# Kernel tuning notes

Hardware: AMD Instinct MI355X
Metric: run time of the kernel (lower is better)

The kernel has to match this reference:

```python
import jax, jax.numpy as jnp
from jax import lax
import numpy as np

B = 8; L = 1024; D_MODEL = 128; N_LAYER = 4
D_INNER = 256; D_STATE = 16; D_CONV = 4; DT_RANK = 8  # ceil(128/16)
N_STATE = 2; EPS = 1e-5


def setup_inputs() -> dict:
    key = jax.random.key(0)
    ks = jax.random.split(key, 9)
    s = 0.02
    return {
        "x": jax.random.normal(ks[0], (B, L, D_MODEL), jnp.float32),
        "in_proj_w": jax.random.normal(ks[1], (N_LAYER, 2 * D_INNER, D_MODEL), jnp.float32) * s,
        "conv_w": jax.random.normal(ks[2], (N_LAYER, D_INNER, 1, D_CONV), jnp.float32) * s,
        "conv_b": jnp.zeros((N_LAYER, D_INNER), jnp.float32),
        "x_proj_w": jax.random.normal(ks[3], (N_LAYER, DT_RANK + 2 * D_STATE, D_INNER), jnp.float32) * s,
        "dt_proj_w": jax.random.normal(ks[4], (N_LAYER, D_INNER, DT_RANK), jnp.float32) * s,
        "dt_proj_b": jax.random.normal(ks[5], (N_LAYER, D_INNER), jnp.float32) * s,
        "A_log": jnp.log(jnp.tile(jnp.arange(1, D_STATE + 1, dtype=jnp.float32), (N_LAYER, D_INNER, 1))),
        "D_param": jnp.ones((N_LAYER, D_INNER), jnp.float32),
        "out_proj_w": jax.random.normal(ks[6], (N_LAYER, D_MODEL, D_INNER), jnp.float32) * s,
        "norm_w": jnp.ones((N_LAYER, D_MODEL), jnp.float32),
        "norm_f_w": jnp.ones((D_MODEL,), jnp.float32),
        "bn_gamma": jnp.ones((D_MODEL,), jnp.float32),
        "bn_beta": jnp.zeros((D_MODEL,), jnp.float32),
        "head_w": jax.random.normal(ks[7], (N_STATE, D_MODEL), jnp.float32) * s,
        "head_b": jnp.zeros((N_STATE,), jnp.float32),
    }


def _rmsnorm(x, w):
    return x * lax.rsqrt(jnp.mean(x * x, axis=-1, keepdims=True) + EPS) * w


def _selective_scan(u, delta, A, Bm, Cm, D):
    # u, delta: (b,l,d); A: (d,n); Bm, Cm: (b,l,n); D: (d,)
    deltaA = jnp.exp(delta[..., None] * A)                          # (b,l,d,n)
    deltaBu = delta[..., None] * Bm[:, :, None, :] * u[..., None]   # (b,l,d,n)

    def step(h, t):
        dA, dBu, c = t
        h = dA * h + dBu                                            # (b,d,n)
        return h, jnp.einsum('bdn,bn->bd', h, c)

    h0 = jnp.zeros((u.shape[0], u.shape[2], A.shape[1]), u.dtype)
    _, ys = lax.scan(step, h0, (jnp.moveaxis(deltaA, 1, 0),
                                jnp.moveaxis(deltaBu, 1, 0),
                                jnp.moveaxis(Cm, 1, 0)))
    return jnp.moveaxis(ys, 0, 1) + u * D                           # (b,l,d)


def _mamba_block(x, in_w, cw, cb, xp_w, dt_w, dt_b, A_log, Dp, out_w):
    xz = jnp.einsum('bld,ed->ble', x, in_w)                         # (b,l,2*d_inner)
    xs, res = jnp.split(xz, 2, axis=-1)
    # depthwise causal conv, kernel D_CONV, left pad D_CONV-1 (matches pad=3 + truncate)
    xc = lax.conv_general_dilated(jnp.transpose(xs, (0, 2, 1)), cw, (1,),
                                  [(D_CONV - 1, 0)],
                                  dimension_numbers=('NCH', 'OIH', 'NCH'),
                                  feature_group_count=D_INNER)
    xs = jax.nn.silu(jnp.transpose(xc + cb[None, :, None], (0, 2, 1)))
    dbc = jnp.einsum('bld,ed->ble', xs, xp_w)
    dlt, Bm, Cm = jnp.split(dbc, [DT_RANK, DT_RANK + D_STATE], axis=-1)
    delta = jax.nn.softplus(jnp.einsum('blr,dr->bld', dlt, dt_w) + dt_b)
    A = -jnp.exp(A_log)
    y = _selective_scan(xs, delta, A, Bm, Cm, Dp)
    y = y * jax.nn.silu(res)
    return jnp.einsum('ble,de->bld', y, out_w)


def reference(x, in_proj_w, conv_w, conv_b, x_proj_w, dt_proj_w, dt_proj_b,
              A_log, D_param, out_proj_w, norm_w, norm_f_w,
              bn_gamma, bn_beta, head_w, head_b):
    h = x
    for i in range(N_LAYER):
        h = h + _mamba_block(_rmsnorm(h, norm_w[i]), in_proj_w[i], conv_w[i],
                             conv_b[i], x_proj_w[i], dt_proj_w[i], dt_proj_b[i],
                             A_log[i], D_param[i], out_proj_w[i])
    h = _rmsnorm(h, norm_f_w)
    feat = h[:, -1, :]                                              # (b, d_model)
    # BatchNorm1d (training mode: batch stats, biased variance), ReLU, Dropout(eval)=id
    mu = jnp.mean(feat, axis=0)
    var = jnp.mean((feat - mu) ** 2, axis=0)
    feat = (feat - mu) * lax.rsqrt(var + EPS) * bn_gamma + bn_beta
    feat = jax.nn.relu(feat)
    return feat @ head_w.T + head_b                                 # (b, n_state)
```

## Files before the change

kernel.cpp:

```cpp
#include <hip/hip_runtime.h>
#include <cstddef>

#define LQ 1024
#define DM 128
#define DI 256
#define DSN 16
#define NB 8
#define ROWS (NB*LQ)
#define EPSF 1e-5f
#define CHUNK 32
#define NCHUNK (LQ/CHUNK)

typedef _Float16 f16;
typedef __attribute__((ext_vector_type(8))) _Float16 f16x8;
typedef __attribute__((ext_vector_type(4))) _Float16 f16x4;
typedef __attribute__((ext_vector_type(4))) float f32x4;

static __device__ __forceinline__ float sigmoid_f(float x) { return 1.f/(1.f+__expf(-x)); }
static __device__ __forceinline__ float softplus_f(float x) {
  return (x > 20.f) ? x : log1pf(__expf(x));
}

__global__ __launch_bounds__(256) void cvt_all(
    const float* __restrict__ a, const float* __restrict__ bsrc, const float* __restrict__ csrc,
    f16* __restrict__ oa, f16* __restrict__ ob, f16* __restrict__ oc)
{
  int i = blockIdx.x*256 + threadIdx.x;
  const int na = (4*2*DI*DM)/4;
  const int nb = (4*40*DI)/4;
  const int nc = (4*DM*DI)/4;
  const float* s; f16* o; int k;
  if (i < na)            { s = a;    o = oa; k = i; }
  else if (i < na+nb)    { s = bsrc; o = ob; k = i - na; }
  else if (i < na+nb+nc) { s = csrc; o = oc; k = i - na - nb; }
  else return;
  float4 v = ((const float4*)s)[k];
  f16x4 r; r.x=(f16)v.x; r.y=(f16)v.y; r.z=(f16)v.z; r.w=(f16)v.w;
  ((f16x4*)o)[k] = r;
}

__global__ __launch_bounds__(256) void norm_inproj(
    const float* __restrict__ hin, const float* __restrict__ nw,
    const f16* __restrict__ Wf, f16* __restrict__ xz)
{
  __shared__ __align__(16) f16 Alds[64][136];
  __shared__ __align__(16) f16 Blds[64][136];
  const int tid = threadIdx.x;
  const int row0 = blockIdx.x*64, col0 = blockIdx.y*64;
  #pragma unroll
  for (int cc = tid; cc < 1024; cc += 256) {
    int r = cc >> 4, off = (cc & 15) << 3;
    *(f16x8*)&Blds[r][off] = *(const f16x8*)(Wf + (size_t)(col0 + r)*DM + off);
  }
  {
    const int r = tid >> 2, seg = (tid & 3) * 32;
    const float* hr = hin + (size_t)(row0 + r)*DM + seg;
    float4 v[8];
    float ss = 0.f;
    #pragma unroll
    for (int j = 0; j < 8; ++j) {
      v[j] = *(const float4*)(hr + j*4);
      ss += v[j].x*v[j].x + v[j].y*v[j].y + v[j].z*v[j].z + v[j].w*v[j].w;
    }
    ss += __shfl_xor(ss, 1);
    ss += __shfl_xor(ss, 2);
    const float sc = rsqrtf(ss*(1.f/128.f) + EPSF);
    #pragma unroll
    for (int j = 0; j < 8; ++j) {
      float4 wv = *(const float4*)(nw + seg + j*4);
      f16x4 o;
      o.x = (f16)(v[j].x*sc*wv.x);
      o.y = (f16)(v[j].y*sc*wv.y);
      o.z = (f16)(v[j].z*sc*wv.z);
      o.w = (f16)(v[j].w*sc*wv.w);
      *(f16x4*)&Alds[r][seg + j*4] = o;
    }
  }
  __syncthreads();
  const int l = tid & 63, w = tid >> 6;
  const int wr = w >> 1, wc = w & 1;
  const int fr = l & 15, kg = l >> 4;
  f16x8 af[2][4], bf[2][4];
  #pragma unroll
  for (int m = 0; m < 2; ++m)
    #pragma unroll
    for (int s = 0; s < 4; ++s)
      af[m][s] = *(const f16x8*)&Alds[wr*32 + m*16 + fr][s*32 + kg*8];
  #pragma unroll
  for (int n = 0; n < 2; ++n)
    #pragma unroll
    for (int s = 0; s < 4; ++s)
      bf[n][s] = *(const f16x8*)&Blds[wc*32 + n*16 + fr][s*32 + kg*8];
  f32x4 acc[2][2];
  #pragma unroll
  for (int m = 0; m < 2; ++m)
    #pragma unroll
    for (int n = 0; n < 2; ++n)
      acc[m][n] = (f32x4){0.f,0.f,0.f,0.f};
  #pragma unroll
  for (int s = 0; s < 4; ++s)
    #pragma unroll
    for (int m = 0; m < 2; ++m)
      #pragma unroll
      for (int n = 0; n < 2; ++n)
        acc[m][n] = __builtin_amdgcn_mfma_f32_16x16x32_f16(af[m][s], bf[n][s], acc[m][n], 0, 0, 0);
  #pragma unroll
  for (int m = 0; m < 2; ++m)
    #pragma unroll
    for (int n = 0; n < 2; ++n) {
      const int col = col0 + wc*32 + n*16 + fr;
      #pragma unroll
      for (int j = 0; j < 4; ++j) {
        const int row = row0 + wr*32 + m*16 + kg*4 + j;
        xz[(size_t)row*(2*DI) + col] = (f16)acc[m][n][j];
      }
    }
}

__global__ __launch_bounds__(256) void conv_xproj_p1(
    const f16* __restrict__ xz, const float* __restrict__ cw, const float* __restrict__ cb,
    const f16* __restrict__ xpw, const float* __restrict__ A_log,
    const float* __restrict__ dtw, const float* __restrict__ dtb,
    f16* __restrict__ xs_out, float* __restrict__ dbc_out,
    float* __restrict__ S, float* __restrict__ sumdl_out)
{
  __shared__ __align__(16) f16 sXz[35][256];
  __shared__ __align__(16) f16 sXs[32][264];
  __shared__ __align__(16) f16 sW[48][264];
  __shared__ __align__(16) float sDbc[32][40];
  const int bc = blockIdx.x;
  const int b = bc >> 5, ck = bc & (NCHUNK-1);
  const int t0 = ck*CHUNK;
  const int tid = threadIdx.x;
  for (int e = tid; e < 35*32; e += 256) {
    int r = e >> 5, off = (e & 31) << 3;
    f16x8 v = (f16x8){0,0,0,0,0,0,0,0};
    if (ck > 0 || r >= 3)
      v = *(const f16x8*)(xz + (size_t)(b*LQ + t0 - 3 + r)*(2*DI) + off);
    *(f16x8*)&sXz[r][off] = v;
  }
  for (int e = tid; e < 48*32; e += 256) {
    int r = e >> 5, off = (e & 31) << 3;
    f16x8 v = (f16x8){0,0,0,0,0,0,0,0};
    if (r < 40) v = *(const f16x8*)(xpw + (size_t)r*DI + off);
    *(f16x8*)&sW[r][off] = v;
  }
  __syncthreads();
  {
    const int d = tid;
    const float4 cwv = *(const float4*)(cw + d*4);
    const float bias = cb[d];
    #pragma unroll 4
    for (int t = 0; t < CHUNK; ++t) {
      float acc = bias + (float)sXz[t][d]*cwv.x + (float)sXz[t+1][d]*cwv.y
                       + (float)sXz[t+2][d]*cwv.z + (float)sXz[t+3][d]*cwv.w;
      float sv = acc * sigmoid_f(acc);
      f16 s16 = (f16)sv;
      sXs[t][d] = s16;
      xs_out[(size_t)(b*LQ + t0 + t)*DI + d] = s16;
    }
  }
  __syncthreads();
  const int l = tid & 63, w = tid >> 6;
  const int fr = l & 15, kg = l >> 4;
  if (w < 3) {
    f32x4 acc[2];
    acc[0] = (f32x4){0.f,0.f,0.f,0.f};
    acc[1] = (f32x4){0.f,0.f,0.f,0.f};
    #pragma unroll
    for (int s = 0; s < 8; ++s) {
      f16x8 bfv = *(const f16x8*)&sW[w*16 + fr][s*32 + kg*8];
      #pragma unroll
      for (int m = 0; m < 2; ++m) {
        f16x8 afv = *(const f16x8*)&sXs[m*16 + fr][s*32 + kg*8];
        acc[m] = __builtin_amdgcn_mfma_f32_16x16x32_f16(afv, bfv, acc[m], 0, 0, 0);
      }
    }
    const int col = w*16 + fr;
    if (col < 40) {
      #pragma unroll
      for (int m = 0; m < 2; ++m)
        #pragma unroll
        for (int j = 0; j < 4; ++j) {
          int row = m*16 + kg*4 + j;
          sDbc[row][col] = acc[m][j];
          dbc_out[(size_t)(b*LQ + t0 + row)*40 + col] = acc[m][j];
        }
    }
  }
  __syncthreads();
  {
    const int d = tid;
    float A[16];
    #pragma unroll
    for (int n = 0; n < 16; ++n) A[n] = -__expf(A_log[d*16+n]);
    const float4 dw0 = *(const float4*)(dtw + d*8);
    const float4 dw1 = *(const float4*)(dtw + d*8 + 4);
    const float bt = dtb[d];
    float h[16] = {};
    float sdl = 0.f;
    for (int t = 0; t < CHUNK; ++t) {
      float xa = bt + sDbc[t][0]*dw0.x + sDbc[t][1]*dw0.y + sDbc[t][2]*dw0.z + sDbc[t][3]*dw0.w
                    + sDbc[t][4]*dw1.x + sDbc[t][5]*dw1.y + sDbc[t][6]*dw1.z + sDbc[t][7]*dw1.w;
      float dl = softplus_f(xa);
      float uu = (float)sXs[t][d];
      float du = dl*uu;
      sdl += dl;
      #pragma unroll
      for (int n = 0; n < 16; ++n)
        h[n] = __expf(dl*A[n])*h[n] + du*sDbc[t][8+n];
    }
    float* Sp = S + ((size_t)bc*DI + d)*16;
    #pragma unroll
    for (int n = 0; n < 16; n += 4)
      *(float4*)(Sp+n) = make_float4(h[n],h[n+1],h[n+2],h[n+3]);
    sumdl_out[(size_t)bc*DI + d] = sdl;
  }
}

__global__ __launch_bounds__(256) void scan_p2(
    float* __restrict__ S, const float* __restrict__ sumdl,
    const float* __restrict__ A_log)
{
  int g = blockIdx.x*256 + threadIdx.x;
  int b = g >> 12;
  int dn = g & 4095;
  float A = -__expf(A_log[dn]);
  int d = dn >> 4;
  float H = 0.f;
  for (int c = 0; c < NCHUNK; ++c) {
    size_t cidx = (size_t)(b*NCHUNK + c)*DI + d;
    size_t idx = cidx*16 + (dn & 15);
    float Sv = S[idx];
    float P = __expf(A * sumdl[cidx]);
    S[idx] = H;
    H = P*H + Sv;
  }
}

__global__ __launch_bounds__(256) void p3_outproj(
    const f16* __restrict__ xs, const float* __restrict__ dbc,
    const float* __restrict__ A_log, const float* __restrict__ dtw,
    const float* __restrict__ dtb, const float* __restrict__ Dp,
    const float* __restrict__ Hinit, const f16* __restrict__ xz,
    const f16* __restrict__ Wo, const float* __restrict__ addsrc,
    float* __restrict__ hout)
{
  __shared__ __align__(16) f16 sY[32][264];
  __shared__ float sB[CHUNK][16];
  __shared__ float sC[CHUNK][16];
  __shared__ float sDL[CHUNK][8];
  const int bc = blockIdx.x;
  const int b = bc >> 5, ck = bc & (NCHUNK-1);
  const int t0 = ck*CHUNK;
  const int tid = threadIdx.x;
  for (int e = tid; e < CHUNK*16; e += 256) {
    int t = e >> 4, n = e & 15;
    size_t r = (size_t)(b*LQ + t0 + t)*40;
    sB[t][n] = dbc[r + 8 + n];
    sC[t][n] = dbc[r + 24 + n];
  }
  for (int e = tid; e < CHUNK*8; e += 256) {
    int t = e >> 3, j = e & 7;
    sDL[t][j] = dbc[(size_t)(b*LQ + t0 + t)*40 + j];
  }
  const int d = tid;
  float A[16];
  #pragma unroll
  for (int n = 0; n < 16; ++n) A[n] = -__expf(A_log[d*16+n]);
  const float4 dw0 = *(const float4*)(dtw + d*8);
  const float4 dw1 = *(const float4*)(dtw + d*8 + 4);
  const float bt = dtb[d];
  const float Dv = Dp[d];
  float h[16];
  const float* Hp = Hinit + ((size_t)bc*DI + d)*16;
  #pragma unroll
  for (int n = 0; n < 16; n += 4) {
    float4 v = *(const float4*)(Hp+n);
    h[n]=v.x; h[n+1]=v.y; h[n+2]=v.z; h[n+3]=v.w;
  }
  __syncthreads();
  const size_t ubase = (size_t)(b*LQ + t0)*DI + d;
  const size_t rbase = (size_t)(b*LQ + t0)*(2*DI) + DI + d;
  for (int t = 0; t < CHUNK; ++t) {
    float xa = bt + sDL[t][0]*dw0.x + sDL[t][1]*dw0.y + sDL[t][2]*dw0.z + sDL[t][3]*dw0.w
                  + sDL[t][4]*dw1.x + sDL[t][5]*dw1.y + sDL[t][6]*dw1.z + sDL[t][7]*dw1.w;
    float dl = softplus_f(xa);
    float uu = (float)xs[ubase + (size_t)t*DI];
    float du = dl*uu;
    float acc = uu*Dv;
    #pragma unroll
    for (int n = 0; n < 16; ++n) {
      h[n] = __expf(dl*A[n])*h[n] + du*sB[t][n];
      acc += h[n]*sC[t][n];
    }
    float res = (float)xz[rbase + (size_t)t*(2*DI)];
    sY[t][d] = (f16)(acc * (res * sigmoid_f(res)));
  }
  __syncthreads();
  const int l = tid & 63, w = tid >> 6;
  const int fr = l & 15, kg = l >> 4;
  f16x8 bf[2][8];
  #pragma unroll
  for (int n = 0; n < 2; ++n)
    #pragma unroll
    for (int s = 0; s < 8; ++s)
      bf[n][s] = *(const f16x8*)(Wo + (size_t)(w*32 + n*16 + fr)*DI + s*32 + kg*8);
  f32x4 acc[2][2];
  #pragma unroll
  for (int m = 0; m < 2; ++m)
    #pragma unroll
    for (int n = 0; n < 2; ++n)
      acc[m][n] = (f32x4){0.f,0.f,0.f,0.f};
  #pragma unroll
  for (int s = 0; s < 8; ++s)
    #pragma unroll
    for (int m = 0; m < 2; ++m) {
      f16x8 afv = *(const f16x8*)&sY[m*16 + fr][s*32 + kg*8];
      #pragma unroll
      for (int n = 0; n < 2; ++n)
        acc[m][n] = __builtin_amdgcn_mfma_f32_16x16x32_f16(afv, bf[n][s], acc[m][n], 0, 0, 0);
    }
  #pragma unroll
  for (int m = 0; m < 2; ++m)
    #pragma unroll
    for (int n = 0; n < 2; ++n) {
      const int col = w*32 + n*16 + fr;
      #pragma unroll
      for (int j = 0; j < 4; ++j) {
        const int row = m*16 + kg*4 + j;
        const size_t gi = (size_t)(b*LQ + t0 + row)*DM + col;
        hout[gi] = acc[m][n][j] + addsrc[gi];
      }
    }
}

__global__ __launch_bounds__(256) void final_kernel(const float* __restrict__ h,
    const float* __restrict__ nfw, const float* __restrict__ gamma, const float* __restrict__ beta,
    const float* __restrict__ hw, const float* __restrict__ hb, float* __restrict__ out) {
  __shared__ float sf[8][128];
  __shared__ float sscale[8];
  int tid = threadIdx.x;
  for (int e = tid; e < 1024; e += 256) {
    int b = e >> 7, dd = e & 127;
    sf[b][dd] = h[((size_t)b*LQ + (LQ-1))*DM + dd];
  }
  __syncthreads();
  if (tid < 8) {
    float ss = 0.f;
    for (int dd = 0; dd < 128; ++dd) { float v = sf[tid][dd]; ss += v*v; }
    sscale[tid] = rsqrtf(ss/128.f + EPSF);
  }
  __syncthreads();
  for (int e = tid; e < 1024; e += 256) {
    int b = e >> 7, dd = e & 127;
    sf[b][dd] = sf[b][dd]*sscale[b]*nfw[dd];
  }
  __syncthreads();
  if (tid < 128) {
    float mu = 0.f;
    for (int b = 0; b < 8; ++b) mu += sf[b][tid];
    mu *= 0.125f;
    float var = 0.f;
    for (int b = 0; b < 8; ++b) { float dv = sf[b][tid]-mu; var += dv*dv; }
    var *= 0.125f;
    float rs = rsqrtf(var + EPSF);
    for (int b = 0; b < 8; ++b) {
      float v = (sf[b][tid]-mu)*rs*gamma[tid] + beta[tid];
      sf[b][tid] = v > 0.f ? v : 0.f;
    }
  }
  __syncthreads();
  if (tid < 16) {
    int b = tid >> 1, s = tid & 1;
    float acc = hb[s];
    for (int dd = 0; dd < 128; ++dd) acc += sf[b][dd]*hw[s*128+dd];
    out[b*2+s] = acc;
  }
}

extern "C" void kernel_launch(void* const* d_in, const int* in_sizes, int n_in,
                              void* d_out, int out_size, void* d_ws, size_t ws_size,
                              hipStream_t stream) {
  const float* x      = (const float*)d_in[0];
  const float* in_w   = (const float*)d_in[1];
  const float* conv_w = (const float*)d_in[2];
  const float* conv_b = (const float*)d_in[3];
  const float* xp_w   = (const float*)d_in[4];
  const float* dt_w   = (const float*)d_in[5];
  const float* dt_b   = (const float*)d_in[6];
  const float* A_log  = (const float*)d_in[7];
  const float* Dp     = (const float*)d_in[8];
  const float* out_w  = (const float*)d_in[9];
  const float* norm_w = (const float*)d_in[10];
  const float* norm_f = (const float*)d_in[11];
  const float* gamma  = (const float*)d_in[12];
  const float* beta   = (const float*)d_in[13];
  const float* head_w = (const float*)d_in[14];
  const float* head_b = (const float*)d_in[15];

  float* ws = (float*)d_ws;
  float* h     = ws;
  float* dbc   = h + (size_t)ROWS*DM;
  float* S     = dbc + (size_t)ROWS*40;
  float* sumdl = S + (size_t)NB*NCHUNK*DI*16;
  f16* xz     = (f16*)(sumdl + (size_t)NB*NCHUNK*DI);
  f16* xs     = xz + (size_t)ROWS*2*DI;
  f16* wf_in  = xs + (size_t)ROWS*DI;
  f16* wf_xp  = wf_in + (size_t)4*2*DI*DM;
  f16* wf_out = wf_xp + (size_t)4*40*DI;

  cvt_all<<<424, 256, 0, stream>>>(in_w, xp_w, out_w, wf_in, wf_xp, wf_out);

  for (int layer = 0; layer < 4; ++layer) {
    const float* src = layer ? h : x;
    norm_inproj<<<dim3(ROWS/64, 8), 256, 0, stream>>>(
        src, norm_w + (size_t)layer*DM, wf_in + (size_t)layer*2*DI*DM, xz);
    conv_xproj_p1<<<NB*NCHUNK, 256, 0, stream>>>(
        xz, conv_w + (size_t)layer*DI*4, conv_b + (size_t)layer*DI,
        wf_xp + (size_t)layer*40*DI, A_log + (size_t)layer*DI*DSN,
        dt_w + (size_t)layer*DI*8, dt_b + (size_t)layer*DI,
        xs, dbc, S, sumdl);
    scan_p2<<<NB*DI*DSN/256, 256, 0, stream>>>(S, sumdl, A_log + (size_t)layer*DI*DSN);
    p3_outproj<<<NB*NCHUNK, 256, 0, stream>>>(
        xs, dbc, A_log + (size_t)layer*DI*DSN, dt_w + (size_t)layer*DI*8,
        dt_b + (size_t)layer*DI, Dp + (size_t)layer*DI, S, xz,
        wf_out + (size_t)layer*DM*DI, src, h);
  }
  final_kernel<<<1, 256, 0, stream>>>(h, norm_f, gamma, beta, head_w, head_b, (float*)d_out);
}
```

Measured before the change: 308.3 us.

## Fuse norm and in-projection into scan kernels and drop the chunk-state pass

The separate norm+in-projection kernel is folded into the per-chunk front kernel, which recomputes the x half of the projection for its 35 rows including the conv halo. The back kernel recomputes the z half from the source rows. This removes the global xz buffer write and read. The scan_p2 kernel is removed: each back block serially combines the chunk-end states of all earlier chunks to build its own initial state. In exchange there is redundant halo and projection compute, a serial loop of up to 31 chunks per block, and fewer, heavier blocks in place of the wide standalone GEMM.

```diff
diff --git a/kernel.cpp b/kernel.cpp
--- a/kernel.cpp
+++ b/kernel.cpp
@@ -39,156 +39,141 @@
   ((f16x4*)o)[k] = r;
 }
 
-__global__ __launch_bounds__(256) void norm_inproj(
-    const float* __restrict__ hin, const float* __restrict__ nw,
-    const f16* __restrict__ Wf, f16* __restrict__ xz)
-{
-  __shared__ __align__(16) f16 Alds[64][136];
-  __shared__ __align__(16) f16 Blds[64][136];
-  const int tid = threadIdx.x;
-  const int row0 = blockIdx.x*64, col0 = blockIdx.y*64;
-  #pragma unroll
-  for (int cc = tid; cc < 1024; cc += 256) {
-    int r = cc >> 4, off = (cc & 15) << 3;
-    *(f16x8*)&Blds[r][off] = *(const f16x8*)(Wf + (size_t)(col0 + r)*DM + off);
-  }
-  {
-    const int r = tid >> 2, seg = (tid & 3) * 32;
-    const float* hr = hin + (size_t)(row0 + r)*DM + seg;
-    float4 v[8];
-    float ss = 0.f;
-    #pragma unroll
-    for (int j = 0; j < 8; ++j) {
-      v[j] = *(const float4*)(hr + j*4);
-      ss += v[j].x*v[j].x + v[j].y*v[j].y + v[j].z*v[j].z + v[j].w*v[j].w;
-    }
-    ss += __shfl_xor(ss, 1);
-    ss += __shfl_xor(ss, 2);
-    const float sc = rsqrtf(ss*(1.f/128.f) + EPSF);
-    #pragma unroll
-    for (int j = 0; j < 8; ++j) {
-      float4 wv = *(const float4*)(nw + seg + j*4);
-      f16x4 o;
-      o.x = (f16)(v[j].x*sc*wv.x);
-      o.y = (f16)(v[j].y*sc*wv.y);
-      o.z = (f16)(v[j].z*sc*wv.z);
-      o.w = (f16)(v[j].w*sc*wv.w);
-      *(f16x4*)&Alds[r][seg + j*4] = o;
-    }
-  }
-  __syncthreads();
-  const int l = tid & 63, w = tid >> 6;
-  const int wr = w >> 1, wc = w & 1;
-  const int fr = l & 15, kg = l >> 4;
-  f16x8 af[2][4], bf[2][4];
-  #pragma unroll
-  for (int m = 0; m < 2; ++m)
-    #pragma unroll
-    for (int s = 0; s < 4; ++s)
-      af[m][s] = *(const f16x8*)&Alds[wr*32 + m*16 + fr][s*32 + kg*8];
-  #pragma unroll
-  for (int n = 0; n < 2; ++n)
-    #pragma unroll
-    for (int s = 0; s < 4; ++s)
-      bf[n][s] = *(const f16x8*)&Blds[wc*32 + n*16 + fr][s*32 + kg*8];
-  f32x4 acc[2][2];
-  #pragma unroll
-  for (int m = 0; m < 2; ++m)
-    #pragma unroll
-    for (int n = 0; n < 2; ++n)
-      acc[m][n] = (f32x4){0.f,0.f,0.f,0.f};
-  #pragma unroll
-  for (int s = 0; s < 4; ++s)
-    #pragma unroll
-    for (int m = 0; m < 2; ++m)
-      #pragma unroll
-      for (int n = 0; n < 2; ++n)
-        acc[m][n] = __builtin_amdgcn_mfma_f32_16x16x32_f16(af[m][s], bf[n][s], acc[m][n], 0, 0, 0);
-  #pragma unroll
-  for (int m = 0; m < 2; ++m)
-    #pragma unroll
-    for (int n = 0; n < 2; ++n) {
-      const int col = col0 + wc*32 + n*16 + fr;
-      #pragma unroll
-      for (int j = 0; j < 4; ++j) {
-        const int row = row0 + wr*32 + m*16 + kg*4 + j;
-        xz[(size_t)row*(2*DI) + col] = (f16)acc[m][n][j];
-      }
-    }
-}
-
-__global__ __launch_bounds__(256) void conv_xproj_p1(
-    const f16* __restrict__ xz, const float* __restrict__ cw, const float* __restrict__ cb,
-    const f16* __restrict__ xpw, const float* __restrict__ A_log,
+__global__ __launch_bounds__(256) void layer_front(
+    const float* __restrict__ src, const float* __restrict__ nw,
+    const f16* __restrict__ Win,
+    const float* __restrict__ cw, const float* __restrict__ cb,
+    const f16* __restrict__ xpw,
+    const float* __restrict__ A_log,
     const float* __restrict__ dtw, const float* __restrict__ dtb,
     f16* __restrict__ xs_out, float* __restrict__ dbc_out,
     float* __restrict__ S, float* __restrict__ sumdl_out)
 {
-  __shared__ __align__(16) f16 sXz[35][256];
+  __shared__ __align__(16) f16 Ah[48][136];
+  __shared__ __align__(16) f16 sXc[48][264];
   __shared__ __align__(16) f16 sXs[32][264];
-  __shared__ __align__(16) f16 sW[48][264];
   __shared__ __align__(16) float sDbc[32][40];
   const int bc = blockIdx.x;
   const int b = bc >> 5, ck = bc & (NCHUNK-1);
   const int t0 = ck*CHUNK;
   const int tid = threadIdx.x;
-  for (int e = tid; e < 35*32; e += 256) {
-    int r = e >> 5, off = (e & 31) << 3;
-    f16x8 v = (f16x8){0,0,0,0,0,0,0,0};
-    if (ck > 0 || r >= 3)
-      v = *(const f16x8*)(xz + (size_t)(b*LQ + t0 - 3 + r)*(2*DI) + off);
-    *(f16x8*)&sXz[r][off] = v;
-  }
-  for (int e = tid; e < 48*32; e += 256) {
-    int r = e >> 5, off = (e & 31) << 3;
-    f16x8 v = (f16x8){0,0,0,0,0,0,0,0};
-    if (r < 40) v = *(const f16x8*)(xpw + (size_t)r*DI + off);
-    *(f16x8*)&sW[r][off] = v;
-  }
-  __syncthreads();
+
+  {
+    const int r = tid >> 2;
+    const int seg = (tid & 3) * 32;
+    float4 v[8];
+    float ss = 0.f;
+    const bool valid = (r < 35) && (ck > 0 || r >= 3);
+    if (valid) {
+      const float* hr = src + (size_t)(b*LQ + t0 - 3 + r)*DM + seg;
+      #pragma unroll
+      for (int j = 0; j < 8; ++j) {
+        v[j] = *(const float4*)(hr + j*4);
+        ss += v[j].x*v[j].x + v[j].y*v[j].y + v[j].z*v[j].z + v[j].w*v[j].w;
+      }
+    }
+    ss += __shfl_xor(ss, 1);
+    ss += __shfl_xor(ss, 2);
+    if (r < 48) {
+      if (valid) {
+        const float sc = rsqrtf(ss*(1.f/128.f) + EPSF);
+        #pragma unroll
+        for (int j = 0; j < 8; ++j) {
+          float4 wv = *(const float4*)(nw + seg + j*4);
+          f16x4 o;
+          o.x=(f16)(v[j].x*sc*wv.x); o.y=(f16)(v[j].y*sc*wv.y);
+          o.z=(f16)(v[j].z*sc*wv.z); o.w=(f16)(v[j].w*sc*wv.w);
+          *(f16x4*)&Ah[r][seg + j*4] = o;
+        }
+      } else {
+        #pragma unroll
+        for (int j = 0; j < 8; ++j)
+          *(f16x4*)&Ah[r][seg + j*4] = (f16x4){0,0,0,0};
+      }
+    }
+  }
+  __syncthreads();
+
+  const int l = tid & 63, w = tid >> 6;
+  const int fr = l & 15, kg = l >> 4;
+
+  {
+    f32x4 acc[3][4];
+    #pragma unroll
+    for (int m = 0; m < 3; ++m)
+      #pragma unroll
+      for (int n = 0; n < 4; ++n)
+        acc[m][n] = (f32x4){0.f,0.f,0.f,0.f};
+    #pragma unroll
+    for (int s = 0; s < 4; ++s) {
+      f16x8 af[3];
+      #pragma unroll
+      for (int m = 0; m < 3; ++m)
+        af[m] = *(const f16x8*)&Ah[m*16 + fr][s*32 + kg*8];
+      #pragma unroll
+      for (int n = 0; n < 4; ++n) {
+        f16x8 bfv = *(const f16x8*)(Win + (size_t)(w*64 + n*16 + fr)*DM + s*32 + kg*8);
+        #pragma unroll
+        for (int m = 0; m < 3; ++m)
+          acc[m][n] = __builtin_amdgcn_mfma_f32_16x16x32_f16(af[m], bfv, acc[m][n], 0, 0, 0);
+      }
+    }
+    #pragma unroll
+    for (int m = 0; m < 3; ++m)
+      #pragma unroll
+      for (int n = 0; n < 4; ++n) {
+        const int col = w*64 + n*16 + fr;
+        #pragma unroll
+        for (int j = 0; j < 4; ++j)
+          sXc[m*16 + kg*4 + j][col] = (f16)acc[m][n][j];
+      }
+  }
+  __syncthreads();
+
   {
     const int d = tid;
     const float4 cwv = *(const float4*)(cw + d*4);
     const float bias = cb[d];
     #pragma unroll 4
     for (int t = 0; t < CHUNK; ++t) {
-      float acc = bias + (float)sXz[t][d]*cwv.x + (float)sXz[t+1][d]*cwv.y
-                       + (float)sXz[t+2][d]*cwv.z + (float)sXz[t+3][d]*cwv.w;
-      float sv = acc * sigmoid_f(acc);
+      float a = bias + (float)sXc[t][d]*cwv.x + (float)sXc[t+1][d]*cwv.y
+                     + (float)sXc[t+2][d]*cwv.z + (float)sXc[t+3][d]*cwv.w;
+      float sv = a * sigmoid_f(a);
       f16 s16 = (f16)sv;
       sXs[t][d] = s16;
       xs_out[(size_t)(b*LQ + t0 + t)*DI + d] = s16;
     }
   }
   __syncthreads();
-  const int l = tid & 63, w = tid >> 6;
-  const int fr = l & 15, kg = l >> 4;
+
   if (w < 3) {
     f32x4 acc[2];
     acc[0] = (f32x4){0.f,0.f,0.f,0.f};
     acc[1] = (f32x4){0.f,0.f,0.f,0.f};
+    const int wrow = w*16 + fr;
     #pragma unroll
     for (int s = 0; s < 8; ++s) {
-      f16x8 bfv = *(const f16x8*)&sW[w*16 + fr][s*32 + kg*8];
+      f16x8 bfv = (f16x8){0,0,0,0,0,0,0,0};
+      if (wrow < 40) bfv = *(const f16x8*)(xpw + (size_t)wrow*DI + s*32 + kg*8);
       #pragma unroll
       for (int m = 0; m < 2; ++m) {
         f16x8 afv = *(const f16x8*)&sXs[m*16 + fr][s*32 + kg*8];
         acc[m] = __builtin_amdgcn_mfma_f32_16x16x32_f16(afv, bfv, acc[m], 0, 0, 0);
       }
     }
-    const int col = w*16 + fr;
-    if (col < 40) {
+    if (wrow < 40) {
       #pragma unroll
       for (int m = 0; m < 2; ++m)
         #pragma unroll
         for (int j = 0; j < 4; ++j) {
           int row = m*16 + kg*4 + j;
-          sDbc[row][col] = acc[m][j];
-          dbc_out[(size_t)(b*LQ + t0 + row)*40 + col] = acc[m][j];
+          sDbc[row][wrow] = acc[m][j];
+          dbc_out[(size_t)(b*LQ + t0 + row)*40 + wrow] = acc[m][j];
         }
     }
   }
   __syncthreads();
+
   {
     const int d = tid;
     float A[16];
@@ -218,34 +203,18 @@
   }
 }
 
-__global__ __launch_bounds__(256) void scan_p2(
-    float* __restrict__ S, const float* __restrict__ sumdl,
-    const float* __restrict__ A_log)
-{
-  int g = blockIdx.x*256 + threadIdx.x;
-  int b = g >> 12;
-  int dn = g & 4095;
-  float A = -__expf(A_log[dn]);
-  int d = dn >> 4;
-  float H = 0.f;
-  for (int c = 0; c < NCHUNK; ++c) {
-    size_t cidx = (size_t)(b*NCHUNK + c)*DI + d;
-    size_t idx = cidx*16 + (dn & 15);
-    float Sv = S[idx];
-    float P = __expf(A * sumdl[cidx]);
-    S[idx] = H;
-    H = P*H + Sv;
-  }
-}
-
-__global__ __launch_bounds__(256) void p3_outproj(
+__global__ __launch_bounds__(256) void layer_back(
+    const float* __restrict__ src, const float* __restrict__ nw,
+    const f16* __restrict__ Win,
     const f16* __restrict__ xs, const float* __restrict__ dbc,
-    const float* __restrict__ A_log, const float* __restrict__ dtw,
-    const float* __restrict__ dtb, const float* __restrict__ Dp,
-    const float* __restrict__ Hinit, const f16* __restrict__ xz,
-    const f16* __restrict__ Wo, const float* __restrict__ addsrc,
+    const float* __restrict__ A_log,
+    const float* __restrict__ dtw, const float* __restrict__ dtb,
+    const float* __restrict__ Dp, const float* __restrict__ S,
+    const float* __restrict__ sumdl, const f16* __restrict__ Wo,
     float* __restrict__ hout)
 {
+  __shared__ __align__(16) f16 Ah[32][136];
+  __shared__ __align__(16) f16 sZ[32][264];
   __shared__ __align__(16) f16 sY[32][264];
   __shared__ float sB[CHUNK][16];
   __shared__ float sC[CHUNK][16];
@@ -254,6 +223,31 @@
   const int b = bc >> 5, ck = bc & (NCHUNK-1);
   const int t0 = ck*CHUNK;
   const int tid = threadIdx.x;
+
+  {
+    const int r = tid >> 3;
+    const int seg = (tid & 7) * 16;
+    const float* hr = src + (size_t)(b*LQ + t0 + r)*DM + seg;
+    float4 v[4];
+    float ss = 0.f;
+    #pragma unroll
+    for (int j = 0; j < 4; ++j) {
+      v[j] = *(const float4*)(hr + j*4);
+      ss += v[j].x*v[j].x + v[j].y*v[j].y + v[j].z*v[j].z + v[j].w*v[j].w;
+    }
+    ss += __shfl_xor(ss, 1);
+    ss += __shfl_xor(ss, 2);
+    ss += __shfl_xor(ss, 4);
+    const float sc = rsqrtf(ss*(1.f/128.f) + EPSF);
+    #pragma unroll
+    for (int j = 0; j < 4; ++j) {
+      float4 wv = *(const float4*)(nw + seg + j*4);
+      f16x4 o;
+      o.x=(f16)(v[j].x*sc*wv.x); o.y=(f16)(v[j].y*sc*wv.y);
+      o.z=(f16)(v[j].z*sc*wv.z); o.w=(f16)(v[j].w*sc*wv.w);
+      *(f16x4*)&Ah[r][seg + j*4] = o;
+    }
+  }
   for (int e = tid; e < CHUNK*16; e += 256) {
     int t = e >> 4, n = e & 15;
     size_t r = (size_t)(b*LQ + t0 + t)*40;
@@ -264,75 +258,121 @@
     int t = e >> 3, j = e & 7;
     sDL[t][j] = dbc[(size_t)(b*LQ + t0 + t)*40 + j];
   }
+  __syncthreads();
+
+  const int l = tid & 63, w = tid >> 6;
+  const int fr = l & 15, kg = l >> 4;
+
+  {
+    f32x4 acc[2][4];
+    #pragma unroll
+    for (int m = 0; m < 2; ++m)
+      #pragma unroll
+      for (int n = 0; n < 4; ++n)
+        acc[m][n] = (f32x4){0.f,0.f,0.f,0.f};
+    #pragma unroll
+    for (int s = 0; s < 4; ++s) {
+      f16x8 af[2];
+      #pragma unroll
+      for (int m = 0; m < 2; ++m)
+        af[m] = *(const f16x8*)&Ah[m*16 + fr][s*32 + kg*8];
+      #pragma unroll
+      for (int n = 0; n < 4; ++n) {
+        f16x8 bfv = *(const f16x8*)(Win + (size_t)(DI + w*64 + n*16 + fr)*DM + s*32 + kg*8);
+        #pragma unroll
+        for (int m = 0; m < 2; ++m)
+          acc[m][n] = __builtin_amdgcn_mfma_f32_16x16x32_f16(af[m], bfv, acc[m][n], 0, 0, 0);
+      }
+    }
+    #pragma unroll
+    for (int m = 0; m < 2; ++m)
+      #pragma unroll
+      for (int n = 0; n < 4; ++n) {
+        const int col = w*64 + n*16 + fr;
+        #pragma unroll
+        for (int j = 0; j < 4; ++j)
+          sZ[m*16 + kg*4 + j][col] = (f16)acc[m][n][j];
+      }
+  }
+
   const int d = tid;
   float A[16];
   #pragma unroll
   for (int n = 0; n < 16; ++n) A[n] = -__expf(A_log[d*16+n]);
+  float h[16] = {};
+  for (int c = 0; c < ck; ++c) {
+    float sdl = sumdl[(size_t)(b*NCHUNK + c)*DI + d];
+    const float* Sp = S + ((size_t)(b*NCHUNK + c)*DI + d)*16;
+    #pragma unroll
+    for (int n = 0; n < 16; n += 4) {
+      float4 sv = *(const float4*)(Sp + n);
+      h[n]   = __expf(A[n]  *sdl)*h[n]   + sv.x;
+      h[n+1] = __expf(A[n+1]*sdl)*h[n+1] + sv.y;
+      h[n+2] = __expf(A[n+2]*sdl)*h[n+2] + sv.z;
+      h[n+3] = __expf(A[n+3]*sdl)*h[n+3] + sv.w;
+    }
+  }
   const float4 dw0 = *(const float4*)(dtw + d*8);
   const float4 dw1 = *(const float4*)(dtw + d*8 + 4);
   const float bt = dtb[d];
   const float Dv = Dp[d];
-  float h[16];
-  const float* Hp = Hinit + ((size_t)bc*DI + d)*16;
-  #pragma unroll
-  for (int n = 0; n < 16; n += 4) {
-    float4 v = *(const float4*)(Hp+n);
-    h[n]=v.x; h[n+1]=v.y; h[n+2]=v.z; h[n+3]=v.w;
-  }
-  __syncthreads();
-  const size_t ubase = (size_t)(b*LQ + t0)*DI + d;
-  const size_t rbase = (size_t)(b*LQ + t0)*(2*DI) + DI + d;
-  for (int t = 0; t < CHUNK; ++t) {
-    float xa = bt + sDL[t][0]*dw0.x + sDL[t][1]*dw0.y + sDL[t][2]*dw0.z + sDL[t][3]*dw0.w
-                  + sDL[t][4]*dw1.x + sDL[t][5]*dw1.y + sDL[t][6]*dw1.z + sDL[t][7]*dw1.w;
-    float dl = softplus_f(xa);
-    float uu = (float)xs[ubase + (size_t)t*DI];
-    float du = dl*uu;
-    float acc = uu*Dv;
-    #pragma unroll
-    for (int n = 0; n < 16; ++n) {
-      h[n] = __expf(dl*A[n])*h[n] + du*sB[t][n];
-      acc += h[n]*sC[t][n];
-    }
-    float res = (float)xz[rbase + (size_t)t*(2*DI)];
-    sY[t][d] = (f16)(acc * (res * sigmoid_f(res)));
-  }
-  __syncthreads();
-  const int l = tid & 63, w = tid >> 6;
-  const int fr = l & 15, kg = l >> 4;
-  f16x8 bf[2][8];
-  #pragma unroll
-  for (int n = 0; n < 2; ++n)
+  __syncthreads();
+
+  {
+    const size_t ubase = (size_t)(b*LQ + t0)*DI + d;
+    for (int t = 0; t < CHUNK; ++t) {
+      float xa = bt + sDL[t][0]*dw0.x + sDL[t][1]*dw0.y + sDL[t][2]*dw0.z + sDL[t][3]*dw0.w
+                    + sDL[t][4]*dw1.x + sDL[t][5]*dw1.y + sDL[t][6]*dw1.z + sDL[t][7]*dw1.w;
+      float dl = softplus_f(xa);
+      float uu = (float)xs[ubase + (size_t)t*DI];
+      float du = dl*uu;
+      float acc = uu*Dv;
+      #pragma unroll
+      for (int n = 0; n < 16; ++n) {
+        h[n] = __expf(dl*A[n])*h[n] + du*sB[t][n];
+        acc += h[n]*sC[t][n];
+      }
+      float res = (float)sZ[t][d];
+      sY[t][d] = (f16)(acc * (res * sigmoid_f(res)));
+    }
+  }
+  __syncthreads();
+
+  {
+    f16x8 bf[2][8];
+    #pragma unroll
+    for (int n = 0; n < 2; ++n)
+      #pragma unroll
+      for (int s = 0; s < 8; ++s)
+        bf[n][s] = *(const f16x8*)(Wo + (size_t)(w*32 + n*16 + fr)*DI + s*32 + kg*8);
+    f32x4 acc[2][2];
+    #pragma unroll
+    for (int m = 0; m < 2; ++m)
+      #pragma unroll
+      for (int n = 0; n < 2; ++n)
+        acc[m][n] = (f32x4){0.f,0.f,0.f,0.f};
     #pragma unroll
     for (int s = 0; s < 8; ++s)
-      bf[n][s] = *(const f16x8*)(Wo + (size_t)(w*32 + n*16 + fr)*DI + s*32 + kg*8);
-  f32x4 acc[2][2];
-  #pragma unroll
-  for (int m = 0; m < 2; ++m)
-    #pragma unroll
-    for (int n = 0; n < 2; ++n)
-      acc[m][n] = (f32x4){0.f,0.f,0.f,0.f};
-  #pragma unroll
-  for (int s = 0; s < 8; ++s)
-    #pragma unroll
-    for (int m = 0; m < 2; ++m) {
-      f16x8 afv = *(const f16x8*)&sY[m*16 + fr][s*32 + kg*8];
-      #pragma unroll
-      for (int n = 0; n < 2; ++n)
-        acc[m][n] = __builtin_amdgcn_mfma_f32_16x16x32_f16(afv, bf[n][s], acc[m][n], 0, 0, 0);
-    }
-  #pragma unroll
-  for (int m = 0; m < 2; ++m)
-    #pragma unroll
-    for (int n = 0; n < 2; ++n) {
-      const int col = w*32 + n*16 + fr;
-      #pragma unroll
-      for (int j = 0; j < 4; ++j) {
-        const int row = m*16 + kg*4 + j;
-        const size_t gi = (size_t)(b*LQ + t0 + row)*DM + col;
-        hout[gi] = acc[m][n][j] + addsrc[gi];
-      }
-    }
+      #pragma unroll
+      for (int m = 0; m < 2; ++m) {
+        f16x8 afv = *(const f16x8*)&sY[m*16 + fr][s*32 + kg*8];
+        #pragma unroll
+        for (int n = 0; n < 2; ++n)
+          acc[m][n] = __builtin_amdgcn_mfma_f32_16x16x32_f16(afv, bf[n][s], acc[m][n], 0, 0, 0);
+      }
+    #pragma unroll
+    for (int m = 0; m < 2; ++m)
+      #pragma unroll
+      for (int n = 0; n < 2; ++n) {
+        const int col = w*32 + n*16 + fr;
+        #pragma unroll
+        for (int j = 0; j < 4; ++j) {
+          const int row = m*16 + kg*4 + j;
+          const size_t gi = (size_t)(b*LQ + t0 + row)*DM + col;
+          hout[gi] = acc[m][n][j] + src[gi];
+        }
+      }
+  }
 }
 
 __global__ __launch_bounds__(256) void final_kernel(const float* __restrict__ h,
@@ -404,8 +444,7 @@
   float* dbc   = h + (size_t)ROWS*DM;
   float* S     = dbc + (size_t)ROWS*40;
   float* sumdl = S + (size_t)NB*NCHUNK*DI*16;
-  f16* xz     = (f16*)(sumdl + (size_t)NB*NCHUNK*DI);
-  f16* xs     = xz + (size_t)ROWS*2*DI;
+  f16* xs     = (f16*)(sumdl + (size_t)NB*NCHUNK*DI);
   f16* wf_in  = xs + (size_t)ROWS*DI;
   f16* wf_xp  = wf_in + (size_t)4*2*DI*DM;
   f16* wf_out = wf_xp + (size_t)4*40*DI;
@@ -414,18 +453,18 @@
 
   for (int layer = 0; layer < 4; ++layer) {
     const float* src = layer ? h : x;
-    norm_inproj<<<dim3(ROWS/64, 8), 256, 0, stream>>>(
-        src, norm_w + (size_t)layer*DM, wf_in + (size_t)layer*2*DI*DM, xz);
-    conv_xproj_p1<<<NB*NCHUNK, 256, 0, stream>>>(
-        xz, conv_w + (size_t)layer*DI*4, conv_b + (size_t)layer*DI,
+    layer_front<<<NB*NCHUNK, 256, 0, stream>>>(
+        src, norm_w + (size_t)layer*DM, wf_in + (size_t)layer*2*DI*DM,
+        conv_w + (size_t)layer*DI*4, conv_b + (size_t)layer*DI,
         wf_xp + (size_t)layer*40*DI, A_log + (size_t)layer*DI*DSN,
         dt_w + (size_t)layer*DI*8, dt_b + (size_t)layer*DI,
         xs, dbc, S, sumdl);
-    scan_p2<<<NB*DI*DSN/256, 256, 0, stream>>>(S, sumdl, A_log + (size_t)layer*DI*DSN);
-    p3_outproj<<<NB*NCHUNK, 256, 0, stream>>>(
-        xs, dbc, A_log + (size_t)layer*DI*DSN, dt_w + (size_t)layer*DI*8,
-        dt_b + (size_t)layer*DI, Dp + (size_t)layer*DI, S, xz,
-        wf_out + (size_t)layer*DM*DI, src, h);
+    layer_back<<<NB*NCHUNK, 256, 0, stream>>>(
+        src, norm_w + (size_t)layer*DM, wf_in + (size_t)layer*2*DI*DM,
+        xs, dbc, A_log + (size_t)layer*DI*DSN,
+        dt_w + (size_t)layer*DI*8, dt_b + (size_t)layer*DI,
+        Dp + (size_t)layer*DI, S, sumdl,
+        wf_out + (size_t)layer*DM*DI, h);
   }
   final_kernel<<<1, 256, 0, stream>>>(h, norm_f, gamma, beta, head_w, head_b, (float*)d_out);
 }
```

New measurement: 313.3 us. About the same (+1.6%).

## Halve scan chunk size to double block count and stage operands in LDS

Applied to the files above, without the earlier changes.

The scan chunk length drops from 32 to 16, so the chunked front and back kernels launch twice as many blocks (512 instead of 256) and each block runs a shorter sequential recurrence. The x_proj weights are read straight from global memory into MFMA operands instead of being staged in shared memory. The back kernel now preloads xs, the z gate and the dt/B/C rows into shared memory with vector loads, replacing strided per-timestep global reads. In exchange, scan_p2 must walk twice as many chunks serially, and the chunk-state buffer grows, but the workspace pointers are derived from NCHUNK and scale with it.

```diff
diff --git a/kernel.cpp b/kernel.cpp
--- a/kernel.cpp
+++ b/kernel.cpp
@@ -8,7 +8,7 @@
 #define NB 8
 #define ROWS (NB*LQ)
 #define EPSF 1e-5f
-#define CHUNK 32
+#define CHUNK 16
 #define NCHUNK (LQ/CHUNK)
 
 typedef _Float16 f16;
@@ -117,78 +117,69 @@
     }
 }
 
-__global__ __launch_bounds__(256) void conv_xproj_p1(
+__global__ __launch_bounds__(256) void layer_front(
     const f16* __restrict__ xz, const float* __restrict__ cw, const float* __restrict__ cb,
     const f16* __restrict__ xpw, const float* __restrict__ A_log,
     const float* __restrict__ dtw, const float* __restrict__ dtb,
     f16* __restrict__ xs_out, float* __restrict__ dbc_out,
     float* __restrict__ S, float* __restrict__ sumdl_out)
 {
-  __shared__ __align__(16) f16 sXz[35][256];
-  __shared__ __align__(16) f16 sXs[32][264];
-  __shared__ __align__(16) f16 sW[48][264];
-  __shared__ __align__(16) float sDbc[32][40];
+  __shared__ __align__(16) f16 sXz[19][264];
+  __shared__ __align__(16) f16 sXs[16][264];
+  __shared__ __align__(16) float sDbc[16][40];
   const int bc = blockIdx.x;
-  const int b = bc >> 5, ck = bc & (NCHUNK-1);
+  const int b = bc >> 6, ck = bc & (NCHUNK-1);
   const int t0 = ck*CHUNK;
   const int tid = threadIdx.x;
-  for (int e = tid; e < 35*32; e += 256) {
+  const int l = tid & 63, w = tid >> 6;
+  const int fr = l & 15, kg = l >> 4;
+
+  for (int e = tid; e < 19*32; e += 256) {
     int r = e >> 5, off = (e & 31) << 3;
     f16x8 v = (f16x8){0,0,0,0,0,0,0,0};
     if (ck > 0 || r >= 3)
       v = *(const f16x8*)(xz + (size_t)(b*LQ + t0 - 3 + r)*(2*DI) + off);
     *(f16x8*)&sXz[r][off] = v;
   }
-  for (int e = tid; e < 48*32; e += 256) {
-    int r = e >> 5, off = (e & 31) << 3;
-    f16x8 v = (f16x8){0,0,0,0,0,0,0,0};
-    if (r < 40) v = *(const f16x8*)(xpw + (size_t)r*DI + off);
-    *(f16x8*)&sW[r][off] = v;
-  }
-  __syncthreads();
+  __syncthreads();
+
   {
     const int d = tid;
     const float4 cwv = *(const float4*)(cw + d*4);
     const float bias = cb[d];
     #pragma unroll 4
     for (int t = 0; t < CHUNK; ++t) {
-      float acc = bias + (float)sXz[t][d]*cwv.x + (float)sXz[t+1][d]*cwv.y
-                       + (float)sXz[t+2][d]*cwv.z + (float)sXz[t+3][d]*cwv.w;
-      float sv = acc * sigmoid_f(acc);
+      float a = bias + (float)sXz[t][d]*cwv.x + (float)sXz[t+1][d]*cwv.y
+                     + (float)sXz[t+2][d]*cwv.z + (float)sXz[t+3][d]*cwv.w;
+      float sv = a * sigmoid_f(a);
       f16 s16 = (f16)sv;
       sXs[t][d] = s16;
       xs_out[(size_t)(b*LQ + t0 + t)*DI + d] = s16;
     }
   }
   __syncthreads();
-  const int l = tid & 63, w = tid >> 6;
-  const int fr = l & 15, kg = l >> 4;
+
   if (w < 3) {
-    f32x4 acc[2];
-    acc[0] = (f32x4){0.f,0.f,0.f,0.f};
-    acc[1] = (f32x4){0.f,0.f,0.f,0.f};
+    const int col = w*16 + fr;
+    f32x4 acc = (f32x4){0.f,0.f,0.f,0.f};
     #pragma unroll
     for (int s = 0; s < 8; ++s) {
-      f16x8 bfv = *(const f16x8*)&sW[w*16 + fr][s*32 + kg*8];
-      #pragma unroll
-      for (int m = 0; m < 2; ++m) {
-        f16x8 afv = *(const f16x8*)&sXs[m*16 + fr][s*32 + kg*8];
-        acc[m] = __builtin_amdgcn_mfma_f32_16x16x32_f16(afv, bfv, acc[m], 0, 0, 0);
+      f16x8 bfv = (f16x8){0,0,0,0,0,0,0,0};
+      if (col < 40) bfv = *(const f16x8*)(xpw + (size_t)col*DI + s*32 + kg*8);
+      f16x8 afv = *(const f16x8*)&sXs[fr][s*32 + kg*8];
+      acc = __builtin_amdgcn_mfma_f32_16x16x32_f16(afv, bfv, acc, 0, 0, 0);
+    }
+    if (col < 40) {
+      #pragma unroll
+      for (int j = 0; j < 4; ++j) {
+        int row = kg*4 + j;
+        sDbc[row][col] = acc[j];
+        dbc_out[(size_t)(b*LQ + t0 + row)*40 + col] = acc[j];
       }
     }
-    const int col = w*16 + fr;
-    if (col < 40) {
-      #pragma unroll
-      for (int m = 0; m < 2; ++m)
-        #pragma unroll
-        for (int j = 0; j < 4; ++j) {
-          int row = m*16 + kg*4 + j;
-          sDbc[row][col] = acc[m][j];
-          dbc_out[(size_t)(b*LQ + t0 + row)*40 + col] = acc[m][j];
-        }
-    }
-  }
-  __syncthreads();
+  }
+  __syncthreads();
+
   {
     const int d = tid;
     float A[16];
@@ -203,8 +194,7 @@
       float xa = bt + sDbc[t][0]*dw0.x + sDbc[t][1]*dw0.y + sDbc[t][2]*dw0.z + sDbc[t][3]*dw0.w
                     + sDbc[t][4]*dw1.x + sDbc[t][5]*dw1.y + sDbc[t][6]*dw1.z + sDbc[t][7]*dw1.w;
       float dl = softplus_f(xa);
-      float uu = (float)sXs[t][d];
-      float du = dl*uu;
+      float du = dl * (float)sXs[t][d];
       sdl += dl;
       #pragma unroll
       for (int n = 0; n < 16; ++n)
@@ -238,7 +228,7 @@
   }
 }
 
-__global__ __launch_bounds__(256) void p3_outproj(
+__global__ __launch_bounds__(256) void layer_back(
     const f16* __restrict__ xs, const float* __restrict__ dbc,
     const float* __restrict__ A_log, const float* __restrict__ dtw,
     const float* __restrict__ dtb, const float* __restrict__ Dp,
@@ -246,93 +236,94 @@
     const f16* __restrict__ Wo, const float* __restrict__ addsrc,
     float* __restrict__ hout)
 {
-  __shared__ __align__(16) f16 sY[32][264];
-  __shared__ float sB[CHUNK][16];
-  __shared__ float sC[CHUNK][16];
-  __shared__ float sDL[CHUNK][8];
+  __shared__ __align__(16) f16 sXs[16][264];
+  __shared__ __align__(16) f16 sZ[16][264];
+  __shared__ __align__(16) f16 sY[16][264];
+  __shared__ __align__(16) float sDbc[16][40];
   const int bc = blockIdx.x;
-  const int b = bc >> 5, ck = bc & (NCHUNK-1);
+  const int b = bc >> 6, ck = bc & (NCHUNK-1);
   const int t0 = ck*CHUNK;
   const int tid = threadIdx.x;
-  for (int e = tid; e < CHUNK*16; e += 256) {
-    int t = e >> 4, n = e & 15;
-    size_t r = (size_t)(b*LQ + t0 + t)*40;
-    sB[t][n] = dbc[r + 8 + n];
-    sC[t][n] = dbc[r + 24 + n];
-  }
-  for (int e = tid; e < CHUNK*8; e += 256) {
-    int t = e >> 3, j = e & 7;
-    sDL[t][j] = dbc[(size_t)(b*LQ + t0 + t)*40 + j];
-  }
+  const int l = tid & 63, w = tid >> 6;
+  const int fr = l & 15, kg = l >> 4;
+
+  {
+    const int r = tid >> 4, col = (tid & 15) * 16;
+    *(f16x8*)&sXs[r][col]   = *(const f16x8*)(xs + (size_t)(b*LQ + t0 + r)*DI + col);
+    *(f16x8*)&sXs[r][col+8] = *(const f16x8*)(xs + (size_t)(b*LQ + t0 + r)*DI + col + 8);
+    *(f16x8*)&sZ[r][col]    = *(const f16x8*)(xz + (size_t)(b*LQ + t0 + r)*(2*DI) + DI + col);
+    *(f16x8*)&sZ[r][col+8]  = *(const f16x8*)(xz + (size_t)(b*LQ + t0 + r)*(2*DI) + DI + col + 8);
+  }
+  for (int e = tid; e < 16*40; e += 256) {
+    int t = e / 40, c = e % 40;
+    sDbc[t][c] = dbc[(size_t)(b*LQ + t0 + t)*40 + c];
+  }
+
   const int d = tid;
   float A[16];
   #pragma unroll
   for (int n = 0; n < 16; ++n) A[n] = -__expf(A_log[d*16+n]);
+  float h[16];
+  {
+    const float* Hp = Hinit + ((size_t)bc*DI + d)*16;
+    #pragma unroll
+    for (int n = 0; n < 16; n += 4) {
+      float4 v = *(const float4*)(Hp+n);
+      h[n]=v.x; h[n+1]=v.y; h[n+2]=v.z; h[n+3]=v.w;
+    }
+  }
   const float4 dw0 = *(const float4*)(dtw + d*8);
   const float4 dw1 = *(const float4*)(dtw + d*8 + 4);
   const float bt = dtb[d];
   const float Dv = Dp[d];
-  float h[16];
-  const float* Hp = Hinit + ((size_t)bc*DI + d)*16;
-  #pragma unroll
-  for (int n = 0; n < 16; n += 4) {
-    float4 v = *(const float4*)(Hp+n);
-    h[n]=v.x; h[n+1]=v.y; h[n+2]=v.z; h[n+3]=v.w;
-  }
-  __syncthreads();
-  const size_t ubase = (size_t)(b*LQ + t0)*DI + d;
-  const size_t rbase = (size_t)(b*LQ + t0)*(2*DI) + DI + d;
-  for (int t = 0; t < CHUNK; ++t) {
-    float xa = bt + sDL[t][0]*dw0.x + sDL[t][1]*dw0.y + sDL[t][2]*dw0.z + sDL[t][3]*dw0.w
-                  + sDL[t][4]*dw1.x + sDL[t][5]*dw1.y + sDL[t][6]*dw1.z + sDL[t][7]*dw1.w;
-    float dl = softplus_f(xa);
-    float uu = (float)xs[ubase + (size_t)t*DI];
-    float du = dl*uu;
-    float acc = uu*Dv;
-    #pragma unroll
-    for (int n = 0; n < 16; ++n) {
-      h[n] = __expf(dl*A[n])*h[n] + du*sB[t][n];
-      acc += h[n]*sC[t][n];
-    }
-    float res = (float)xz[rbase + (size_t)t*(2*DI)];
-    sY[t][d] = (f16)(acc * (res * sigmoid_f(res)));
-  }
-  __syncthreads();
-  const int l = tid & 63, w = tid >> 6;
-  const int fr = l & 15, kg = l >> 4;
+
   f16x8 bf[2][8];
   #pragma unroll
   for (int n = 0; n < 2; ++n)
     #pragma unroll
     for (int s = 0; s < 8; ++s)
       bf[n][s] = *(const f16x8*)(Wo + (size_t)(w*32 + n*16 + fr)*DI + s*32 + kg*8);
-  f32x4 acc[2][2];
-  #pragma unroll
-  for (int m = 0; m < 2; ++m)
-    #pragma unroll
-    for (int n = 0; n < 2; ++n)
-      acc[m][n] = (f32x4){0.f,0.f,0.f,0.f};
-  #pragma unroll
-  for (int s = 0; s < 8; ++s)
-    #pragma unroll
-    for (int m = 0; m < 2; ++m) {
-      f16x8 afv = *(const f16x8*)&sY[m*16 + fr][s*32 + kg*8];
+  __syncthreads();
+
+  for (int t = 0; t < CHUNK; ++t) {
+    float xa = bt + sDbc[t][0]*dw0.x + sDbc[t][1]*dw0.y + sDbc[t][2]*dw0.z + sDbc[t][3]*dw0.w
+                  + sDbc[t][4]*dw1.x + sDbc[t][5]*dw1.y + sDbc[t][6]*dw1.z + sDbc[t][7]*dw1.w;
+    float dl = softplus_f(xa);
+    float uu = (float)sXs[t][d];
+    float du = dl*uu;
+    float pacc = uu*Dv;
+    #pragma unroll
+    for (int n = 0; n < 16; ++n) {
+      h[n] = __expf(dl*A[n])*h[n] + du*sDbc[t][8+n];
+      pacc += h[n]*sDbc[t][24+n];
+    }
+    float res = (float)sZ[t][d];
+    sY[t][d] = (f16)(pacc * (res * sigmoid_f(res)));
+  }
+  __syncthreads();
+
+  {
+    f32x4 acc[2];
+    acc[0] = (f32x4){0.f,0.f,0.f,0.f};
+    acc[1] = (f32x4){0.f,0.f,0.f,0.f};
+    #pragma unroll
+    for (int s = 0; s < 8; ++s) {
+      f16x8 afv = *(const f16x8*)&sY[fr][s*32 + kg*8];
       #pragma unroll
       for (int n = 0; n < 2; ++n)
-        acc[m][n] = __builtin_amdgcn_mfma_f32_16x16x32_f16(afv, bf[n][s], acc[m][n], 0, 0, 0);
-    }
-  #pragma unroll
-  for (int m = 0; m < 2; ++m)
+        acc[n] = __builtin_amdgcn_mfma_f32_16x16x32_f16(afv, bf[n][s], acc[n], 0, 0, 0);
+    }
     #pragma unroll
     for (int n = 0; n < 2; ++n) {
       const int col = w*32 + n*16 + fr;
       #pragma unroll
       for (int j = 0; j < 4; ++j) {
-        const int row = m*16 + kg*4 + j;
+        const int row = kg*4 + j;
         const size_t gi = (size_t)(b*LQ + t0 + row)*DM + col;
-        hout[gi] = acc[m][n][j] + addsrc[gi];
+        hout[gi] = acc[n][j] + addsrc[gi];
       }
     }
+  }
 }
 
 __global__ __launch_bounds__(256) void final_kernel(const float* __restrict__ h,
@@ -416,13 +407,13 @@
     const float* src = layer ? h : x;
     norm_inproj<<<dim3(ROWS/64, 8), 256, 0, stream>>>(
         src, norm_w + (size_t)layer*DM, wf_in + (size_t)layer*2*DI*DM, xz);
-    conv_xproj_p1<<<NB*NCHUNK, 256, 0, stream>>>(
+    layer_front<<<NB*NCHUNK, 256, 0, stream>>>(
         xz, conv_w + (size_t)layer*DI*4, conv_b + (size_t)layer*DI,
         wf_xp + (size_t)layer*40*DI, A_log + (size_t)layer*DI*DSN,
         dt_w + (size_t)layer*DI*8, dt_b + (size_t)layer*DI,
         xs, dbc, S, sumdl);
     scan_p2<<<NB*DI*DSN/256, 256, 0, stream>>>(S, sumdl, A_log + (size_t)layer*DI*DSN);
-    p3_outproj<<<NB*NCHUNK, 256, 0, stream>>>(
+    layer_back<<<NB*NCHUNK, 256, 0, stream>>>(
         xs, dbc, A_log + (size_t)layer*DI*DSN, dt_w + (size_t)layer*DI*8,
         dt_b + (size_t)layer*DI, Dp + (size_t)layer*DI, S, xz,
         wf_out + (size_t)layer*DM*DI, src, h);
```

Result: faster. 285.3 us (-7.5%).
